# Performance work log

Measured on AMD Instinct MI355X. Metric: run time of the kernel, lower is better.

Reference implementation:

```python
import math
import jax, jax.numpy as jnp
import numpy as np

# Constants (module-level in original repo; plausible biological values)
LATENCY_EPSILON = 1e-6
HAIR_CELL_COMPRESSION_EXPONENT = 0.3
HAIR_CELL_ADAPTATION_SUPPRESSION = 0.5
AUDITORY_NERVE_ADAPTATION_DECAY = 0.9
AUDITORY_NERVE_ADAPTATION_RATE = 0.1

SAMPLE_RATE = 16000
N_FFT = 512
N_FILTERS = 128
OUTPUT_SIZE = 262144
N_TIMESTEPS = 128
SPARSITY = 0.05
F_MIN, F_MAX = 80.0, 7600.0


def build_filterbank() -> np.ndarray:
    """Mel triangular filterbank, faithful to _create_filterbank (integer bin edges)."""
    hz_to_mel = lambda hz: 2595.0 * math.log10(1.0 + hz / 700.0)
    mel_to_hz = lambda mel: 700.0 * (10.0 ** (mel / 2595.0) - 1.0)
    mel_pts = np.linspace(hz_to_mel(F_MIN), hz_to_mel(F_MAX), N_FILTERS + 2)
    hz_pts = np.array([mel_to_hz(m) for m in mel_pts])
    bins = (hz_pts * N_FFT / SAMPLE_RATE).astype(np.int64)  # .long() truncation
    fb = np.zeros((N_FILTERS, N_FFT // 2 + 1), dtype=np.float32)
    for i in range(N_FILTERS):
        l, c, r = bins[i], bins[i + 1], bins[i + 2]
        for j in range(l, c):
            if c > l:
                fb[i, j] = (j - l) / (c - l)
        for j in range(c, r):
            if r > c:
                fb[i, j] = (r - j) / (r - c)
    return fb


def setup_inputs() -> dict:
    key = jax.random.key(0)
    k_audio, k_w = jax.random.split(key)
    audio = jax.random.normal(k_audio, (SAMPLE_RATE,), dtype=jnp.float32)
    filterbank = jnp.asarray(build_filterbank())  # [n_filters, n_fft//2+1]
    W = jax.random.normal(k_w, (OUTPUT_SIZE, N_FILTERS), dtype=jnp.float32) * 0.02
    b = jnp.zeros((OUTPUT_SIZE,), dtype=jnp.float32)
    adaptation_state = jnp.zeros((N_FILTERS,), dtype=jnp.float32)
    return {"audio": audio, "filterbank": filterbank, "W": W, "b": b,
            "adaptation_state": adaptation_state}


def reference(audio, filterbank, W, b, adaptation_state):
    # Basilar membrane: rfft with n=N_FFT (truncates audio to first N_FFT samples)
    spec = jnp.fft.rfft(audio, n=N_FFT)            # [n_fft//2+1] complex
    magnitude = jnp.abs(spec).astype(jnp.float32)   # [257]
    cochlear = filterbank @ magnitude               # [n_filters]
    # Hair cell compression
    hair = jnp.power(cochlear + LATENCY_EPSILON, HAIR_CELL_COMPRESSION_EXPONENT)
    adapted = jax.nn.relu(hair - adaptation_state * HAIR_CELL_ADAPTATION_SUPPRESSION)
    # Output projection (torch Linear: x @ W.T + b)
    activity = W @ adapted + b                      # [output_size]
    # Latency coding: high activity -> early spike (vectorized scatter)
    a_min, a_max = activity.min(), activity.max()
    norm = (activity - a_min) / (a_max - a_min + 1e-6)
    latencies = ((1.0 - norm) * (N_TIMESTEPS - 1)).astype(jnp.int32)  # [output_size]
    fire = norm > SPARSITY                           # [output_size]
    # spikes[t, n] = fire[n] and latencies[n] == t
    spikes = (latencies[None, :] == jnp.arange(N_TIMESTEPS, dtype=jnp.int32)[:, None]) \
             & fire[None, :]                         # [n_timesteps, output_size] bool
    return spikes
```

## Files before the change

kernel.cpp:

```cpp
#include <hip/hip_runtime.h>
#include <math.h>

#ifndef M_PI
#define M_PI 3.14159265358979323846
#endif

#define N_FFT       512
#define N_BINS      257
#define N_FILTERS   128
#define OUTPUT_SIZE 262144
#define N_TIMESTEPS 128

typedef int int4v __attribute__((ext_vector_type(4)));

__device__ __forceinline__ unsigned long long enc_d(double f) {
    unsigned long long u = (unsigned long long)__double_as_longlong(f);
    return (u & 0x8000000000000000ull) ? ~u : (u | 0x8000000000000000ull);
}
__device__ __forceinline__ double dec_d(unsigned long long e) {
    unsigned long long u = (e & 0x8000000000000000ull) ? (e ^ 0x8000000000000000ull) : ~e;
    return __longlong_as_double((long long)u);
}

__global__ __launch_bounds__(64) void k1a_dft(
    const float* __restrict__ audio, float* __restrict__ mag,
    unsigned long long* __restrict__ minmax)
{
    __shared__ double sre[64];
    __shared__ double sim[64];

    const int b    = blockIdx.x;
    const int lane = threadIdx.x;

    double re = 0.0, im = 0.0;
    #pragma unroll
    for (int j = 0; j < 8; ++j) {
        const int n = lane * 8 + j;
        const int m = (b * n) & (N_FFT - 1);
        double s, c;
        sincos((-2.0 * M_PI * (double)m) / (double)N_FFT, &s, &c);
        const double a = (double)audio[n];
        re += a * c;
        im += a * s;
    }
    sre[lane] = re;
    sim[lane] = im;
    __syncthreads();
    #pragma unroll
    for (int s = 32; s > 0; s >>= 1) {
        if (lane < s) {
            sre[lane] += sre[lane + s];
            sim[lane] += sim[lane + s];
        }
        __syncthreads();
    }
    if (lane == 0) {
        mag[b] = (float)sqrt(sre[0] * sre[0] + sim[0] * sim[0]);
        if (b == 0) {
            minmax[0] = 0xFFFFFFFFFFFFFFFFull;
            minmax[1] = 0ull;
        }
    }
}

__global__ __launch_bounds__(256) void k2_gemv(
    const float4* __restrict__ W4, const float* __restrict__ bias,
    const float* __restrict__ fb, const float* __restrict__ mag,
    const float* __restrict__ adapt, double* __restrict__ activity,
    unsigned long long* __restrict__ minmax)
{
    __shared__ float  magl[N_BINS];
    __shared__ double ad[N_FILTERS];
    __shared__ double red_min[256];
    __shared__ double red_max[256];

    const int tid = threadIdx.x;

    for (int j = tid; j < N_BINS; j += 256) magl[j] = mag[j];
    __syncthreads();

    if (tid < N_FILTERS) {
        double acc = 0.0;
        const float* row = fb + tid * N_BINS;
        #pragma unroll 4
        for (int j = 0; j < N_BINS; ++j)
            acc += (double)row[j] * (double)magl[j];
        const double x = acc + 1e-6;
        const double p = pow(x, 0.3);
        const double a = p - (double)adapt[tid] * 0.5;
        ad[tid] = a > 0.0 ? a : 0.0;
    }
    __syncthreads();

    const int row = blockIdx.x * 256 + tid;
    const float4* wrow = W4 + (size_t)row * (N_FILTERS / 4);

    double acc = 0.0;
    #pragma unroll 8
    for (int j = 0; j < N_FILTERS / 4; ++j) {
        float4 w = wrow[j];
        const int k = j * 4;
        acc += (double)w.x * ad[k];
        acc += (double)w.y * ad[k + 1];
        acc += (double)w.z * ad[k + 2];
        acc += (double)w.w * ad[k + 3];
    }
    double a = acc + (double)bias[row];
    activity[row] = a;

    red_min[tid] = a;
    red_max[tid] = a;
    __syncthreads();
    for (int s = 128; s > 0; s >>= 1) {
        if (tid < s) {
            red_min[tid] = fmin(red_min[tid], red_min[tid + s]);
            red_max[tid] = fmax(red_max[tid], red_max[tid + s]);
        }
        __syncthreads();
    }
    if (tid == 0) {
        atomicMin(&minmax[0], enc_d(red_min[0]));
        atomicMax(&minmax[1], enc_d(red_max[0]));
    }
}

__global__ __launch_bounds__(256) void k3_spikes(
    const double* __restrict__ activity,
    const unsigned long long* __restrict__ minmax,
    int4v* __restrict__ out4)
{
    const int tid = blockIdx.x * 256 + threadIdx.x;
    const double amin = dec_d(minmax[0]);
    const double amax = dec_d(minmax[1]);
    const double denom = (amax - amin) + 1e-6;

    const double nx = (activity[4 * tid + 0] - amin) / denom;
    const double ny = (activity[4 * tid + 1] - amin) / denom;
    const double nz = (activity[4 * tid + 2] - amin) / denom;
    const double nw = (activity[4 * tid + 3] - amin) / denom;

    const int lx = (int)((1.0 - nx) * 127.0);
    const int ly = (int)((1.0 - ny) * 127.0);
    const int lz = (int)((1.0 - nz) * 127.0);
    const int lw = (int)((1.0 - nw) * 127.0);

    const int vx = (nx > 0.05) ? 1 : 0;
    const int vy = (ny > 0.05) ? 1 : 0;
    const int vz = (nz > 0.05) ? 1 : 0;
    const int vw = (nw > 0.05) ? 1 : 0;

    const int t0 = blockIdx.y * (N_TIMESTEPS / 4);
    #pragma unroll 8
    for (int t = t0; t < t0 + N_TIMESTEPS / 4; ++t) {
        int4v v;
        v.x = (lx == t) ? vx : 0;
        v.y = (ly == t) ? vy : 0;
        v.z = (lz == t) ? vz : 0;
        v.w = (lw == t) ? vw : 0;
        out4[(size_t)t * (OUTPUT_SIZE / 4) + tid] = v;
    }
}

extern "C" void kernel_launch(void* const* d_in, const int* in_sizes, int n_in,
                              void* d_out, int out_size, void* d_ws, size_t ws_size,
                              hipStream_t stream) {
    (void)in_sizes; (void)n_in; (void)out_size; (void)ws_size;

    const float* audio = (const float*)d_in[0];
    const float* fb    = (const float*)d_in[1];
    const float* W     = (const float*)d_in[2];
    const float* bias  = (const float*)d_in[3];
    const float* adapt = (const float*)d_in[4];
    int* out = (int*)d_out;

    double* activity = (double*)d_ws;
    unsigned long long* minmax =
        (unsigned long long*)(activity + OUTPUT_SIZE);
    float* mag = (float*)(minmax + 2);

    k1a_dft<<<N_BINS, 64, 0, stream>>>(audio, mag, minmax);
    k2_gemv<<<OUTPUT_SIZE / 256, 256, 0, stream>>>(
        (const float4*)W, bias, fb, mag, adapt, activity, minmax);
    k3_spikes<<<dim3(OUTPUT_SIZE / 4 / 256, 4), 256, 0, stream>>>(
        activity, minmax, (int4v*)out);
}
```

Baseline: 304.7 us.

## Hoist filterbank stage into its own kernel and coalesce GEMV with wave shuffles

The filterbank dot product, power compression and adaptation were recomputed by every GEMV block. They now run once in a separate single-block kernel that writes the adapted vector to workspace. The GEMV is restructured so each half-wave reads one 512-byte W row as contiguous float4s, which makes the loads coalesced. Partial sums and the min/max reduction are combined with cross-lane shuffles instead of shared-memory trees. This costs one extra kernel launch and depends on the row-to-lane mapping being right.

```diff
diff --git a/kernel.cpp b/kernel.cpp
--- a/kernel.cpp
+++ b/kernel.cpp
@@ -63,17 +63,11 @@
     }
 }
 
-__global__ __launch_bounds__(256) void k2_gemv(
-    const float4* __restrict__ W4, const float* __restrict__ bias,
+__global__ __launch_bounds__(256) void k1b_post(
     const float* __restrict__ fb, const float* __restrict__ mag,
-    const float* __restrict__ adapt, double* __restrict__ activity,
-    unsigned long long* __restrict__ minmax)
-{
-    __shared__ float  magl[N_BINS];
-    __shared__ double ad[N_FILTERS];
-    __shared__ double red_min[256];
-    __shared__ double red_max[256];
-
+    const float* __restrict__ adapt, double* __restrict__ adapted)
+{
+    __shared__ float magl[N_BINS];
     const int tid = threadIdx.x;
 
     for (int j = tid; j < N_BINS; j += 256) magl[j] = mag[j];
@@ -88,39 +82,62 @@
         const double x = acc + 1e-6;
         const double p = pow(x, 0.3);
         const double a = p - (double)adapt[tid] * 0.5;
-        ad[tid] = a > 0.0 ? a : 0.0;
-    }
+        adapted[tid] = a > 0.0 ? a : 0.0;
+    }
+}
+
+__global__ __launch_bounds__(256) void k2_gemv(
+    const float4* __restrict__ W4, const float* __restrict__ bias,
+    const double* __restrict__ adapted, double* __restrict__ activity,
+    unsigned long long* __restrict__ minmax)
+{
+    __shared__ double ad[N_FILTERS];
+    const int tid  = threadIdx.x;
+    const int lane = tid & 63;
+    const int half = lane >> 5;
+    const int c    = lane & 31;
+
+    if (tid < N_FILTERS) ad[tid] = adapted[tid];
     __syncthreads();
 
-    const int row = blockIdx.x * 256 + tid;
-    const float4* wrow = W4 + (size_t)row * (N_FILTERS / 4);
-
-    double acc = 0.0;
-    #pragma unroll 8
-    for (int j = 0; j < N_FILTERS / 4; ++j) {
-        float4 w = wrow[j];
-        const int k = j * 4;
-        acc += (double)w.x * ad[k];
-        acc += (double)w.y * ad[k + 1];
-        acc += (double)w.z * ad[k + 2];
-        acc += (double)w.w * ad[k + 3];
-    }
-    double a = acc + (double)bias[row];
-    activity[row] = a;
-
-    red_min[tid] = a;
-    red_max[tid] = a;
-    __syncthreads();
-    for (int s = 128; s > 0; s >>= 1) {
-        if (tid < s) {
-            red_min[tid] = fmin(red_min[tid], red_min[tid + s]);
-            red_max[tid] = fmax(red_max[tid], red_max[tid + s]);
-        }
-        __syncthreads();
-    }
-    if (tid == 0) {
-        atomicMin(&minmax[0], enc_d(red_min[0]));
-        atomicMax(&minmax[1], enc_d(red_max[0]));
+    const double A0 = ad[4 * c + 0];
+    const double A1 = ad[4 * c + 1];
+    const double A2 = ad[4 * c + 2];
+    const double A3 = ad[4 * c + 3];
+
+    const int baseRow = (blockIdx.x * 4 + (tid >> 6)) * 16;
+
+    double part[8];
+    #pragma unroll
+    for (int i = 0; i < 8; ++i) {
+        const float4 w = W4[(size_t)(baseRow + 2 * i) * 32 + lane];
+        part[i] = (double)w.x * A0 + (double)w.y * A1
+                + (double)w.z * A2 + (double)w.w * A3;
+    }
+
+    #pragma unroll
+    for (int off = 1; off < 32; off <<= 1) {
+        #pragma unroll
+        for (int i = 0; i < 8; ++i)
+            part[i] += __shfl_xor(part[i], off);
+    }
+
+    double mn = 1e300, mx = -1e300;
+    if (c < 8) {
+        const int row = baseRow + 2 * c + half;
+        const double a = part[c] + (double)bias[row];
+        activity[row] = a;
+        mn = a;
+        mx = a;
+    }
+    #pragma unroll
+    for (int off = 1; off < 64; off <<= 1) {
+        mn = fmin(mn, __shfl_xor(mn, off));
+        mx = fmax(mx, __shfl_xor(mx, off));
+    }
+    if (lane == 0) {
+        atomicMin(&minmax[0], enc_d(mn));
+        atomicMax(&minmax[1], enc_d(mx));
     }
 }
 
@@ -177,10 +194,12 @@
     unsigned long long* minmax =
         (unsigned long long*)(activity + OUTPUT_SIZE);
     float* mag = (float*)(minmax + 2);
+    double* adapted = (double*)(mag + 512);
 
     k1a_dft<<<N_BINS, 64, 0, stream>>>(audio, mag, minmax);
-    k2_gemv<<<OUTPUT_SIZE / 256, 256, 0, stream>>>(
-        (const float4*)W, bias, fb, mag, adapt, activity, minmax);
+    k1b_post<<<1, 256, 0, stream>>>(fb, mag, adapt, adapted);
+    k2_gemv<<<OUTPUT_SIZE / 64, 256, 0, stream>>>(
+        (const float4*)W, bias, adapted, activity, minmax);
     k3_spikes<<<dim3(OUTPUT_SIZE / 4 / 256, 4), 256, 0, stream>>>(
         activity, minmax, (int4v*)out);
 }
```

New measurement: 636.1 us. 2.09x slower.
